# Kernel tuning notes

Hardware: AMD Instinct MI355X
Metric: run time of the kernel (lower is better)

## Reference

```python
import jax, jax.numpy as jnp
import numpy as np

VOCAB, EMB, HID, OUT = 50257, 256, 512, 4
SEQ, BATCH = 512, 256


def setup_inputs() -> dict:
    key = jax.random.key(0)
    ks = jax.random.split(key, 8)
    text = jax.random.randint(ks[0], (SEQ, BATCH), 0, VOCAB, dtype=jnp.int64)
    s_e = 1.0  # torch Embedding default init is N(0,1)
    emb = jax.random.normal(ks[1], (VOCAB, EMB), dtype=jnp.float32) * s_e
    k_rnn = 1.0 / np.sqrt(HID)  # torch RNN init U(-1/sqrt(H), 1/sqrt(H))
    W_ih = jax.random.uniform(ks[2], (HID, EMB), jnp.float32, -k_rnn, k_rnn)
    W_hh = jax.random.uniform(ks[3], (HID, HID), jnp.float32, -k_rnn, k_rnn)
    b_ih = jax.random.uniform(ks[4], (HID,), jnp.float32, -k_rnn, k_rnn)
    b_hh = jax.random.uniform(ks[5], (HID,), jnp.float32, -k_rnn, k_rnn)
    k_fc = 1.0 / np.sqrt(HID)
    fc_w = jax.random.uniform(ks[6], (OUT, HID), jnp.float32, -k_fc, k_fc)
    fc_b = jax.random.uniform(ks[7], (OUT,), jnp.float32, -k_fc, k_fc)
    return {"text": text, "emb": emb, "W_ih": W_ih, "W_hh": W_hh,
            "b_ih": b_ih, "b_hh": b_hh, "fc_w": fc_w, "fc_b": fc_b}


def reference(text, emb, W_ih, W_hh, b_ih, b_hh, fc_w, fc_b):
    # embedding lookup: [S, B] -> [S, B, E]
    embedded = emb[text]
    # precompute input contribution for all timesteps: [S, B, H]
    x_proj = jnp.einsum('sbe,he->sbh', embedded, W_ih) + b_ih + b_hh

    def step(h, xp):
        h_new = jnp.tanh(xp + h @ W_hh.T)  # [B, H]
        return h_new, None

    h0 = jnp.zeros((text.shape[1], W_hh.shape[0]), dtype=embedded.dtype)
    h_last, _ = jax.lax.scan(step, h0, x_proj)
    # final linear head on last hidden state: [B, OUT]
    return h_last @ fc_w.T + fc_b
```

## Files before the change

### kernel.cpp

```cpp
#include <hip/hip_runtime.h>
#include <hip/hip_bf16.h>
#include <stdint.h>

#define SEQ   512
#define BATCH 256
#define EMBD  256
#define HID   512
#define OUTD  4

typedef float  f32x4 __attribute__((ext_vector_type(4)));
typedef short  s16x8 __attribute__((ext_vector_type(8)));
typedef __bf16 bf16x8 __attribute__((ext_vector_type(8)));

static __device__ __forceinline__ short f2bf(float f) {
    union { float f; uint32_t u; } v; v.f = f;
    uint32_t u = v.u;
    u += 0x7fffu + ((u >> 16) & 1u);
    return (short)(u >> 16);
}
static __device__ __forceinline__ float bf2f(short s) {
    union { uint32_t u; float f; } v;
    v.u = ((uint32_t)(uint16_t)s) << 16;
    return v.f;
}

static __device__ __forceinline__ f32x4 mfma_bf16(s16x8 a, s16x8 b, f32x4 c) {
    return __builtin_amdgcn_mfma_f32_16x16x32_bf16(
        __builtin_bit_cast(bf16x8, a), __builtin_bit_cast(bf16x8, b), c, 0, 0, 0);
}

static __device__ __forceinline__ s16x8 load_coherent_b128(const void* p) {
    s16x8 r;
    asm volatile("global_load_dwordx4 %0, %1, off sc0 sc1"
                 : "=v"(r) : "v"(p) : "memory");
    return r;
}
static __device__ __forceinline__ void store_coherent_b128(void* p, s16x8 v) {
    asm volatile("global_store_dwordx4 %0, %1, off sc0 sc1"
                 :: "v"(p), "v"(v) : "memory");
}
static __device__ __forceinline__ void wait_vm0() {
    asm volatile("s_waitcnt vmcnt(0)" ::: "memory");
    __builtin_amdgcn_sched_barrier(0);
}

static __device__ __forceinline__ void  xp_store(float* p, float v) { *p = v; }
static __device__ __forceinline__ void  xp_store(short* p, float v) { *p = f2bf(v); }
static __device__ __forceinline__ float xp_load(const float* p)     { return *p; }
static __device__ __forceinline__ float xp_load(const short* p)     { return bf2f(*p); }

template <typename XT>
__global__ __launch_bounds__(512, 1)
void xproj_kernel(const int* __restrict__ text, const float* __restrict__ emb,
                  const float* __restrict__ W_ih, const float* __restrict__ b_ih,
                  const float* __restrict__ b_hh, XT* __restrict__ xp) {
    extern __shared__ char lds[];
    char* As = lds;
    char* Bs = lds + 65536;

    const int t    = threadIdx.x;
    const int row0 = blockIdx.x * 128;
    const int col0 = blockIdx.y * 128;

    {
        const int r   = t >> 2;
        const int kc  = (t & 3) * 64;
        const int tok = text[row0 + r];
        const float* src = emb + (size_t)tok * EMBD + kc;
        #pragma unroll
        for (int u = 0; u < 64; u += 8) {
            f32x4 x0 = *(const f32x4*)(src + u);
            f32x4 x1 = *(const f32x4*)(src + u + 4);
            s16x8 pk;
            pk[0]=f2bf(x0.x); pk[1]=f2bf(x0.y); pk[2]=f2bf(x0.z); pk[3]=f2bf(x0.w);
            pk[4]=f2bf(x1.x); pk[5]=f2bf(x1.y); pk[6]=f2bf(x1.z); pk[7]=f2bf(x1.w);
            int byte = (r * 512 + (kc + u) * 2) ^ ((r & 7) << 4);
            *(s16x8*)(As + byte) = pk;
        }
    }
    {
        const int c  = t >> 2;
        const int kc = (t & 3) * 64;
        const float* src = W_ih + (size_t)(col0 + c) * EMBD + kc;
        #pragma unroll
        for (int u = 0; u < 64; u += 8) {
            f32x4 x0 = *(const f32x4*)(src + u);
            f32x4 x1 = *(const f32x4*)(src + u + 4);
            s16x8 pk;
            pk[0]=f2bf(x0.x); pk[1]=f2bf(x0.y); pk[2]=f2bf(x0.z); pk[3]=f2bf(x0.w);
            pk[4]=f2bf(x1.x); pk[5]=f2bf(x1.y); pk[6]=f2bf(x1.z); pk[7]=f2bf(x1.w);
            int byte = (c * 512 + (kc + u) * 2) ^ ((c & 7) << 4);
            *(s16x8*)(Bs + byte) = pk;
        }
    }
    __syncthreads();

    const int lane = t & 63;
    const int w    = t >> 6;
    const int wm   = w >> 2;
    const int wn   = w & 3;
    const int lr   = lane & 15;
    const int lk   = (lane >> 4) * 8;

    f32x4 acc[4][2] = {};
    #pragma unroll
    for (int kk = 0; kk < 8; ++kk) {
        s16x8 a[4], b[2];
        #pragma unroll
        for (int mt = 0; mt < 4; ++mt) {
            int r = wm * 64 + mt * 16 + lr;
            int byte = (r * 512 + (kk * 32 + lk) * 2) ^ ((r & 7) << 4);
            a[mt] = *(const s16x8*)(As + byte);
        }
        #pragma unroll
        for (int nt = 0; nt < 2; ++nt) {
            int c = wn * 32 + nt * 16 + lr;
            int byte = (c * 512 + (kk * 32 + lk) * 2) ^ ((c & 7) << 4);
            b[nt] = *(const s16x8*)(Bs + byte);
        }
        #pragma unroll
        for (int mt = 0; mt < 4; ++mt)
            #pragma unroll
            for (int nt = 0; nt < 2; ++nt)
                acc[mt][nt] = mfma_bf16(a[mt], b[nt], acc[mt][nt]);
    }

    #pragma unroll
    for (int nt = 0; nt < 2; ++nt) {
        const int c = col0 + wn * 32 + nt * 16 + lr;
        const float bias = b_ih[c] + b_hh[c];
        #pragma unroll
        for (int mt = 0; mt < 4; ++mt) {
            #pragma unroll
            for (int r4 = 0; r4 < 4; ++r4) {
                const int rr = row0 + wm * 64 + mt * 16 + (lane >> 4) * 4 + r4;
                xp_store(xp + (size_t)rr * HID + c, acc[mt][nt][r4] + bias);
            }
        }
    }
}

template <typename XT>
__global__ __launch_bounds__(256, 1)
void rnn_kernel(const float* __restrict__ W_hh, const XT* __restrict__ xp,
                const float* __restrict__ fc_w, const float* __restrict__ fc_b,
                short* __restrict__ hbuf, unsigned int* __restrict__ bar,
                float* __restrict__ out) {
    extern __shared__ char lds[];
    short* hstage = (short*)(lds + 131072);

    const int bid  = blockIdx.x;
    const int gi   = (bid & 7) + ((bid >> 5) << 3);
    const int gj   = (bid >> 3) & 3;
    const int t    = threadIdx.x;
    const int lane = t & 63;
    const int w    = t >> 6;
    const int row0 = gi * 16;
    const int col0 = gj * 128;

    {
        const int c  = t >> 1;
        const int k0 = (t & 1) * 256;
        const float* src = W_hh + (size_t)(col0 + c) * HID + k0;
        #pragma unroll 4
        for (int u = 0; u < 256; u += 8) {
            f32x4 x0 = *(const f32x4*)(src + u);
            f32x4 x1 = *(const f32x4*)(src + u + 4);
            s16x8 pk;
            pk[0]=f2bf(x0.x); pk[1]=f2bf(x0.y); pk[2]=f2bf(x0.z); pk[3]=f2bf(x0.w);
            pk[4]=f2bf(x1.x); pk[5]=f2bf(x1.y); pk[6]=f2bf(x1.z); pk[7]=f2bf(x1.w);
            int byte = (c * 1024 + (k0 + u) * 2) ^ ((c & 7) << 4);
            *(s16x8*)(lds + byte) = pk;
        }
    }
    __syncthreads();

    const int lr    = lane & 15;
    const int lkb   = (lane >> 4) * 16;
    const int arow  = row0 + lr;
    const int crow0 = row0 + (lane >> 4) * 4;
    unsigned int* mybar = bar + gi;

    int p = 0;
    for (int s = 0; s < SEQ; ++s) {
        f32x4 acc[2];
        #pragma unroll
        for (int nt = 0; nt < 2; ++nt) {
            const int c = col0 + w * 32 + nt * 16 + lr;
            const XT* xs = xp + ((size_t)s * BATCH + crow0) * HID + c;
            #pragma unroll
            for (int r = 0; r < 4; ++r) acc[nt][r] = xp_load(xs + (size_t)r * HID);
        }

        if (s > 0) {
            if (t == 0) {
                const unsigned int target = 4u * (unsigned int)s;
                int guard = 0;
                while (__hip_atomic_load(mybar, __ATOMIC_RELAXED,
                                         __HIP_MEMORY_SCOPE_AGENT) < target) {
                    __builtin_amdgcn_s_sleep(1);
                    if (++guard > (1 << 27)) break;
                }
            }
            __syncthreads();
        }

        const short* hb   = hbuf + (size_t)p * (BATCH * HID);
        const char*  hrow = (const char*)(hb + (size_t)arow * HID);
        s16x8 areg[16];
        #pragma unroll
        for (int kk = 0; kk < 16; ++kk)
            areg[kk] = load_coherent_b128(hrow + kk * 64 + lkb);
        wait_vm0();

        const int cl0 = w * 32 + lr;
        const int cl1 = cl0 + 16;
        #pragma unroll
        for (int kk = 0; kk < 16; ++kk) {
            const int b0b = (cl0 * 1024 + kk * 64 + lkb) ^ ((cl0 & 7) << 4);
            const int b1b = (cl1 * 1024 + kk * 64 + lkb) ^ ((cl1 & 7) << 4);
            const s16x8 b0v = *(const s16x8*)(lds + b0b);
            const s16x8 b1v = *(const s16x8*)(lds + b1b);
            acc[0] = mfma_bf16(areg[kk], b0v, acc[0]);
            acc[1] = mfma_bf16(areg[kk], b1v, acc[1]);
        }

        #pragma unroll
        for (int nt = 0; nt < 2; ++nt) {
            const int cl = w * 32 + nt * 16 + lr;
            #pragma unroll
            for (int r = 0; r < 4; ++r)
                hstage[((crow0 - row0) + r) * 128 + cl] = f2bf(tanhf(acc[nt][r]));
        }
        __syncthreads();

        {
            const int rr = t >> 4, c8 = (t & 15) * 8;
            s16x8 v = *(const s16x8*)(hstage + rr * 128 + c8);
            short* hn = hbuf + (size_t)(p ^ 1) * (BATCH * HID)
                             + (size_t)(row0 + rr) * HID + (col0 + c8);
            store_coherent_b128(hn, v);
        }
        __syncthreads();

        if (t == 0)
            __hip_atomic_fetch_add(mybar, 1u, __ATOMIC_RELAXED,
                                   __HIP_MEMORY_SCOPE_AGENT);
        p ^= 1;
    }

    if (gj == 0) {
        if (t == 0) {
            int guard = 0;
            while (__hip_atomic_load(mybar, __ATOMIC_RELAXED,
                                     __HIP_MEMORY_SCOPE_AGENT) < 4u * SEQ) {
                __builtin_amdgcn_s_sleep(1);
                if (++guard > (1 << 27)) break;
            }
        }
        __syncthreads();

        const int i  = t >> 2;
        const int q  = t & 3;
        const int bl = i >> 2;
        const int o  = i & 3;
        const short* hb = hbuf + (size_t)p * (BATCH * HID)
                               + (size_t)(row0 + bl) * HID + q * 128;
        s16x8 hv[16];
        #pragma unroll
        for (int kk = 0; kk < 16; ++kk)
            hv[kk] = load_coherent_b128((const char*)hb + kk * 16);
        wait_vm0();
        float sum = 0.f;
        #pragma unroll
        for (int kk = 0; kk < 16; ++kk)
            #pragma unroll
            for (int j = 0; j < 8; ++j)
                sum += bf2f(hv[kk][j]) * fc_w[o * HID + q * 128 + kk * 8 + j];
        sum += __shfl_xor(sum, 1);
        sum += __shfl_xor(sum, 2);
        if (q == 0)
            out[(row0 + bl) * OUTD + o] = sum + fc_b[o];
    }
}

extern "C" void kernel_launch(void* const* d_in, const int* in_sizes, int n_in,
                              void* d_out, int out_size, void* d_ws, size_t ws_size,
                              hipStream_t stream) {
    (void)in_sizes; (void)n_in; (void)out_size;
    const int*   text = (const int*)  d_in[0];
    const float* emb  = (const float*)d_in[1];
    const float* W_ih = (const float*)d_in[2];
    const float* W_hh = (const float*)d_in[3];
    const float* b_ih = (const float*)d_in[4];
    const float* b_hh = (const float*)d_in[5];
    const float* fc_w = (const float*)d_in[6];
    const float* fc_b = (const float*)d_in[7];
    float* out = (float*)d_out;

    char* ws = (char*)d_ws;
    short*        hbuf = (short*)ws;
    unsigned int* bar  = (unsigned int*)(ws + (512 << 10));
    void*         xpbf = (void*)(ws + (1 << 20));

    const size_t base     = (size_t)1 << 20;
    const size_t xp_elems = (size_t)SEQ * BATCH * HID;
    const bool use_f32  = ws_size >= base + xp_elems * 4;
    const bool use_bf16 = !use_f32 && ws_size >= base + xp_elems * 2;

    hipMemsetAsync(ws, 0, (512 << 10) + 4096, stream);

    if (use_f32) {
        hipFuncSetAttribute(reinterpret_cast<const void*>(&xproj_kernel<float>),
                            hipFuncAttributeMaxDynamicSharedMemorySize, 131072);
        hipFuncSetAttribute(reinterpret_cast<const void*>(&rnn_kernel<float>),
                            hipFuncAttributeMaxDynamicSharedMemorySize, 135168);
        xproj_kernel<float><<<dim3(1024, 4, 1), 512, 131072, stream>>>(
            text, emb, W_ih, b_ih, b_hh, (float*)xpbf);
        rnn_kernel<float><<<64, 256, 135168, stream>>>(
            W_hh, (const float*)xpbf, fc_w, fc_b, hbuf, bar, out);
    } else if (use_bf16) {
        hipFuncSetAttribute(reinterpret_cast<const void*>(&xproj_kernel<short>),
                            hipFuncAttributeMaxDynamicSharedMemorySize, 131072);
        hipFuncSetAttribute(reinterpret_cast<const void*>(&rnn_kernel<short>),
                            hipFuncAttributeMaxDynamicSharedMemorySize, 135168);
        xproj_kernel<short><<<dim3(1024, 4, 1), 512, 131072, stream>>>(
            text, emb, W_ih, b_ih, b_hh, (short*)xpbf);
        rnn_kernel<short><<<64, 256, 135168, stream>>>(
            W_hh, (const short*)xpbf, fc_w, fc_b, hbuf, bar, out);
    }
}
```

Before: 2.305 ms.

## Store input projection in bf16 with a packed per-lane layout for the RNN loop

Drops the fp32 input-projection buffer path and always stores x_proj as bf16. The values are written in a permuted layout so that each lane's per-step loads in the recurrent kernel fall close together. The aim is to cut the per-step global traffic and latency of reading x_proj inside the serial recurrence. In exchange the projection is rounded to bf16, and the scattered 2-byte stores in the projection kernel may be less coalesced.

```diff
diff --git a/kernel.cpp b/kernel.cpp
--- a/kernel.cpp
+++ b/kernel.cpp
@@ -44,16 +44,17 @@
     __builtin_amdgcn_sched_barrier(0);
 }
 
-static __device__ __forceinline__ void  xp_store(float* p, float v) { *p = v; }
-static __device__ __forceinline__ void  xp_store(short* p, float v) { *p = f2bf(v); }
-static __device__ __forceinline__ float xp_load(const float* p)     { return *p; }
-static __device__ __forceinline__ float xp_load(const short* p)     { return bf2f(*p); }
-
-template <typename XT>
+static __device__ __forceinline__ size_t xp_pidx(int s, int b, int c) {
+    const int w   = c >> 6, rem = c & 63;
+    const int u   = w * 64 + (((rem & 15) >> 2) << 4) + (b & 15);
+    return ((size_t)(s * 16 + (b >> 4)) * 512 + u) * 16
+           + ((rem >> 4) << 2) + (rem & 3);
+}
+
 __global__ __launch_bounds__(512, 1)
 void xproj_kernel(const int* __restrict__ text, const float* __restrict__ emb,
                   const float* __restrict__ W_ih, const float* __restrict__ b_ih,
-                  const float* __restrict__ b_hh, XT* __restrict__ xp) {
+                  const float* __restrict__ b_hh, short* __restrict__ xp) {
     extern __shared__ char lds[];
     char* As = lds;
     char* Bs = lds + 65536;
@@ -134,15 +135,14 @@
             #pragma unroll
             for (int r4 = 0; r4 < 4; ++r4) {
                 const int rr = row0 + wm * 64 + mt * 16 + (lane >> 4) * 4 + r4;
-                xp_store(xp + (size_t)rr * HID + c, acc[mt][nt][r4] + bias);
+                xp[xp_pidx(rr >> 8, rr & 255, c)] = f2bf(acc[mt][nt][r4] + bias);
             }
         }
     }
 }
 
-template <typename XT>
 __global__ __launch_bounds__(256, 1)
-void rnn_kernel(const float* __restrict__ W_hh, const XT* __restrict__ xp,
+void rnn_kernel(const float* __restrict__ W_hh, const short* __restrict__ xp,
                 const float* __restrict__ fc_w, const float* __restrict__ fc_b,
                 short* __restrict__ hbuf, unsigned int* __restrict__ bar,
                 float* __restrict__ out) {
@@ -187,9 +187,9 @@
         #pragma unroll
         for (int nt = 0; nt < 2; ++nt) {
             const int c = col0 + w * 32 + nt * 16 + lr;
-            const XT* xs = xp + ((size_t)s * BATCH + crow0) * HID + c;
-            #pragma unroll
-            for (int r = 0; r < 4; ++r) acc[nt][r] = xp_load(xs + (size_t)r * HID);
+            #pragma unroll
+            for (int r = 0; r < 4; ++r)
+                acc[nt][r] = bf2f(xp[xp_pidx(s, crow0 + r, c)]);
         }
 
         if (s > 0) {
@@ -301,32 +301,19 @@
     char* ws = (char*)d_ws;
     short*        hbuf = (short*)ws;
     unsigned int* bar  = (unsigned int*)(ws + (512 << 10));
-    void*         xpbf = (void*)(ws + (1 << 20));
-
-    const size_t base     = (size_t)1 << 20;
-    const size_t xp_elems = (size_t)SEQ * BATCH * HID;
-    const bool use_f32  = ws_size >= base + xp_elems * 4;
-    const bool use_bf16 = !use_f32 && ws_size >= base + xp_elems * 2;
+    short*        xpbf = (short*)(ws + (1 << 20));
+    const size_t xp_bytes = (size_t)SEQ * BATCH * HID * 2;
+    const size_t need = ((size_t)1 << 20) + xp_bytes;
+    if (ws_size < need) return;
 
     hipMemsetAsync(ws, 0, (512 << 10) + 4096, stream);
 
-    if (use_f32) {
-        hipFuncSetAttribute(reinterpret_cast<const void*>(&xproj_kernel<float>),
-                            hipFuncAttributeMaxDynamicSharedMemorySize, 131072);
-        hipFuncSetAttribute(reinterpret_cast<const void*>(&rnn_kernel<float>),
-                            hipFuncAttributeMaxDynamicSharedMemorySize, 135168);
-        xproj_kernel<float><<<dim3(1024, 4, 1), 512, 131072, stream>>>(
-            text, emb, W_ih, b_ih, b_hh, (float*)xpbf);
-        rnn_kernel<float><<<64, 256, 135168, stream>>>(
-            W_hh, (const float*)xpbf, fc_w, fc_b, hbuf, bar, out);
-    } else if (use_bf16) {
-        hipFuncSetAttribute(reinterpret_cast<const void*>(&xproj_kernel<short>),
-                            hipFuncAttributeMaxDynamicSharedMemorySize, 131072);
-        hipFuncSetAttribute(reinterpret_cast<const void*>(&rnn_kernel<short>),
-                            hipFuncAttributeMaxDynamicSharedMemorySize, 135168);
-        xproj_kernel<short><<<dim3(1024, 4, 1), 512, 131072, stream>>>(
-            text, emb, W_ih, b_ih, b_hh, (short*)xpbf);
-        rnn_kernel<short><<<64, 256, 135168, stream>>>(
-            W_hh, (const short*)xpbf, fc_w, fc_b, hbuf, bar, out);
-    }
-}
+    hipFuncSetAttribute(reinterpret_cast<const void*>(&xproj_kernel),
+                        hipFuncAttributeMaxDynamicSharedMemorySize, 131072);
+    hipFuncSetAttribute(reinterpret_cast<const void*>(&rnn_kernel),
+                        hipFuncAttributeMaxDynamicSharedMemorySize, 135168);
+    xproj_kernel<<<dim3(1024, 4, 1), 512, 131072, stream>>>(
+        text, emb, W_ih, b_ih, b_hh, xpbf);
+    rnn_kernel<<<64, 256, 135168, stream>>>(
+        W_hh, xpbf, fc_w, fc_b, hbuf, bar, out);
+}
```

Result: no change. 2.343 ms (+1.6%).
